# Kernel tuning notes

Hardware: AMD Instinct MI355X
Metric: run time of the kernel (lower is better)

## Reference

```python
import jax, jax.numpy as jnp
import numpy as np


def setup_inputs() -> dict:
    key = jax.random.key(0)
    k1, k2, k3, k4 = jax.random.split(key, 4)
    N, F_in, F_out = 8192, 512, 256
    inp = jax.random.normal(k1, (N, F_in), dtype=jnp.float32)
    adj = jax.random.uniform(k2, (N, N), dtype=jnp.float32)
    stdv = 1.0 / np.sqrt(F_out)
    weight = jax.random.uniform(k3, (F_in, F_out), minval=-stdv, maxval=stdv, dtype=jnp.float32)
    b = jax.random.uniform(k4, (F_out,), minval=-stdv, maxval=stdv, dtype=jnp.float32)
    return {"input": inp, "adj": adj, "weight": weight, "b": b}


def reference(input, adj, weight, b):
    N = adj.shape[0]
    degree = jnp.sum(adj, axis=1)                      # [N]
    # A_tilde = 2*I - adj
    A_tilde = 2.0 * jnp.eye(N, dtype=adj.dtype) - adj
    d_inv_sqrt = 1.0 / jnp.sqrt(2.0 + degree)          # [N]
    # D^-1/2 @ A_tilde @ D^-1/2 as broadcasted row/col scaling (same math, O(N^2))
    L_sharpen = d_inv_sqrt[:, None] * A_tilde * d_inv_sqrt[None, :]
    support = input @ weight                           # [N, F_out]
    out = L_sharpen @ support + b                      # [N, F_out]
    return jax.nn.relu(out)
```

## Files before the change

kernel.cpp:

```cpp
#include <hip/hip_runtime.h>


typedef _Float16 h4 __attribute__((ext_vector_type(4)));
typedef _Float16 h8 __attribute__((ext_vector_type(8)));
typedef float f4 __attribute__((ext_vector_type(4)));

__device__ __forceinline__ void gload_lds16(const void* g, void* l) {
    __builtin_amdgcn_global_load_lds(
        (const __attribute__((address_space(1))) void*)g,
        (__attribute__((address_space(3))) void*)l, 16, 0, 0);
}

__device__ __forceinline__ void gload2(const float* p, f4& x, f4& y) {
    asm volatile("global_load_dwordx4 %0, %2, off\n\t"
                 "global_load_dwordx4 %1, %2, off offset:16"
                 : "=&v"(x), "=&v"(y)
                 : "v"(p)
                 : "memory");
}
__device__ __forceinline__ void gloadB2(const char* p, h8& x, h8& y) {
    asm volatile("global_load_dwordx4 %0, %2, off\n\t"
                 "global_load_dwordx4 %1, %2, off offset:64"
                 : "=&v"(x), "=&v"(y)
                 : "v"(p)
                 : "memory");
}

__global__ __launch_bounds__(256) void k0_wt(const float* __restrict__ weight,
                                             char* __restrict__ wt) {
    const int idx = blockIdx.x * 256 + threadIdx.x;
    const int k = idx >> 8, j = idx & 255;
    const _Float16 h = (_Float16)weight[idx];
    const int off = j * 1024 + ((k >> 6) << 7) + (((k & 63) << 1) ^ ((j & 7) << 4));
    *(_Float16*)(wt + off) = h;
}

__global__ __launch_bounds__(256) void k1_deg(const float* __restrict__ adj,
                                              float* __restrict__ dinv) {
    const int r = blockIdx.x;
    const float4* rp = (const float4*)(adj + (size_t)r * 8192);
    const int t = threadIdx.x;
    float s = 0.f;
#pragma unroll
    for (int i = 0; i < 8; ++i) {
        float4 v = rp[t + i * 256];
        s += (v.x + v.y) + (v.z + v.w);
    }
#pragma unroll
    for (int off = 32; off > 0; off >>= 1) s += __shfl_down(s, off, 64);
    __shared__ float part[4];
    if ((t & 63) == 0) part[t >> 6] = s;
    __syncthreads();
    if (t == 0) {
        float deg = (part[0] + part[1]) + (part[2] + part[3]);
        dinv[r] = 1.0f / sqrtf(2.0f + deg);
    }
}

__global__ __launch_bounds__(512) void k2_support(const float* __restrict__ input,
                                                  const char* __restrict__ wt,
                                                  const float* __restrict__ dinv,
                                                  char* __restrict__ sT) {
    __shared__ char smem[4096 + 32768];
    const int t = threadIdx.x, w = t >> 6, l = t & 63;
    const int r0 = (int)blockIdx.x * 32;
    const int arow = t >> 4, ak4 = t & 15;
    const int bj = l >> 3, bb = (l & 7) * 16;

    f4 acc[2][2] = {};

    for (int kt = 0; kt < 8; ++kt) {
        const int k0 = kt * 64;
        __syncthreads();
        {
            float4 v = *(const float4*)(input + (size_t)(r0 + arow) * 512 + k0 + ak4 * 4);
            h4 h;
            h[0] = (_Float16)v.x; h[1] = (_Float16)v.y;
            h[2] = (_Float16)v.z; h[3] = (_Float16)v.w;
            *(h4*)(smem + arow * 128 + ((ak4 * 8) ^ ((arow & 7) << 4))) = h;
        }
#pragma unroll
        for (int q = 0; q < 4; ++q) {
            const int c = q * 8 + w;
            gload_lds16(wt + (size_t)(c * 8 + bj) * 1024 + kt * 128 + bb,
                        smem + 4096 + c * 1024);
        }
        __syncthreads();
#pragma unroll
        for (int kk = 0; kk < 2; ++kk) {
            const int ko = kk * 64 + ((l >> 4) << 4);
            h8 a[2], b[2];
#pragma unroll
            for (int m = 0; m < 2; ++m) {
                const int r = m * 16 + (l & 15);
                a[m] = *(const h8*)(smem + r * 128 + (ko ^ ((r & 7) << 4)));
            }
#pragma unroll
            for (int n = 0; n < 2; ++n) {
                const int j = w * 32 + n * 16 + (l & 15);
                b[n] = *(const h8*)(smem + 4096 + j * 128 + (ko ^ ((j & 7) << 4)));
            }
#pragma unroll
            for (int m = 0; m < 2; ++m)
#pragma unroll
                for (int n = 0; n < 2; ++n)
                    acc[m][n] = __builtin_amdgcn_mfma_f32_16x16x32_f16(a[m], b[n], acc[m][n], 0, 0, 0);
        }
    }
#pragma unroll
    for (int m = 0; m < 2; ++m)
#pragma unroll
        for (int n = 0; n < 2; ++n) {
            const int j = w * 32 + n * 16 + (l & 15);
            const int k0r = r0 + m * 16 + ((l >> 4) << 2);
            h4 h;
#pragma unroll
            for (int r = 0; r < 4; ++r)
                h[r] = (_Float16)(dinv[k0r + r] * acc[m][n][r]);
            *(h4*)(sT + (size_t)j * 16384 + (size_t)k0r * 2) = h;
        }
}

__global__ __launch_bounds__(512, 4) void k3_spmm(const float* __restrict__ adj,
                                                  const char* __restrict__ sT,
                                                  float* __restrict__ part,
                                                  float* __restrict__ out,
                                                  int steps) {
    __shared__ __align__(16) char smem[2][8192];
    const int t = threadIdx.x;
    const int w = t >> 6, l = t & 63;
    const int i0 = (int)blockIdx.x * 64;
    const int ks0 = (int)blockIdx.y * steps * 64;
    const int dkt = (i0 - ks0) >> 6;

    const int arow = t >> 3;
    const int ak8 = (t & 7) * 8;
    const int arow_g = i0 + arow;
    const float* aptr = adj + (size_t)arow_g * 8192 + ks0 + ak8;
    const int a_off = arow * 128 + (((t & 7) << 4) ^ ((arow & 7) << 4));

    const char* bp0 = sT + ((size_t)(w * 32 + (l & 15)) * 8192 + ks0 + ((l >> 4) << 3)) * 2;
    const char* bp1 = bp0 + (size_t)16 * 16384;

    f4 acc[4][2] = {};
    h8 bv[2][2];
    f4 ax0, ay0, ax1, ay1;

    auto loadB = [&](int kt) {
        gloadB2(bp0 + (size_t)kt * 128, bv[0][0], bv[1][0]);
        gloadB2(bp1 + (size_t)kt * 128, bv[0][1], bv[1][1]);
    };
    auto waitB = [&]() {
    };
    auto writeA = [&](char* buf, int kt, const f4 x, const f4 y) {
        const int kg = ks0 + kt * 64 + ak8;
        h8 h;
        if (kt == dkt) {
#pragma unroll
            for (int e = 0; e < 4; ++e)
                h[e] = (_Float16)((arow_g == kg + e) ? 2.0f - x[e] : -x[e]);
#pragma unroll
            for (int e = 0; e < 4; ++e)
                h[4 + e] = (_Float16)((arow_g == kg + 4 + e) ? 2.0f - y[e] : -y[e]);
        } else {
#pragma unroll
            for (int e = 0; e < 4; ++e) h[e] = (_Float16)(-x[e]);
#pragma unroll
            for (int e = 0; e < 4; ++e) h[4 + e] = (_Float16)(-y[e]);
        }
        *(h8*)(buf + a_off) = h;
    };
    auto compute = [&](const char* A) {
#pragma unroll
        for (int kk = 0; kk < 2; ++kk) {
            const int ko = kk * 64 + ((l >> 4) << 4);
            h8 a[4];
#pragma unroll
            for (int m = 0; m < 4; ++m) {
                const int r = m * 16 + (l & 15);
                a[m] = *(const h8*)(A + r * 128 + (ko ^ ((r & 7) << 4)));
            }
#pragma unroll
            for (int m = 0; m < 4; ++m)
#pragma unroll
                for (int n = 0; n < 2; ++n)
                    acc[m][n] = __builtin_amdgcn_mfma_f32_16x16x32_f16(a[m], bv[kk][n], acc[m][n], 0, 0, 0);
        }
    };

#define WAIT_ADJ(N, X, Y)                                                     \
    asm volatile("s_waitcnt vmcnt(" #N ")" : "+v"(X), "+v"(Y) :: "memory");   \
    __builtin_amdgcn_sched_barrier(0);
#define WAIT_B(N)                                                             \
    asm volatile("s_waitcnt vmcnt(" #N ")"                                    \
                 : "+v"(bv[0][0]), "+v"(bv[0][1]), "+v"(bv[1][0]), "+v"(bv[1][1]) \
                 :: "memory");                                                \
    __builtin_amdgcn_sched_barrier(0);
#define BARRIER()                                                             \
    asm volatile("s_waitcnt lgkmcnt(0)\n\ts_barrier" ::: "memory");           \
    __builtin_amdgcn_sched_barrier(0);

    gload2(aptr, ax0, ay0);
    gload2(aptr + 64, ax1, ay1);
    WAIT_ADJ(2, ax0, ay0)
    writeA(smem[0], 0, ax0, ay0);
    BARRIER()

#define BODY(kt, XC, YC, XN, YN, BUFC, BUFN)                                  \
    {                                                                         \
        loadB(kt);                                                            \
        gload2(aptr + (size_t)(kt + 2) * 64, XC, YC);                         \
        WAIT_ADJ(6, XN, YN)                                                   \
        writeA(BUFN, (kt) + 1, XN, YN);                                       \
        WAIT_B(2)                                                             \
        compute(BUFC);                                                        \
        BARRIER()                                                             \
    }

    for (int kt2 = 0; kt2 + 3 <= steps; kt2 += 2) {
        BODY(kt2,     ax0, ay0, ax1, ay1, smem[0], smem[1])
        BODY(kt2 + 1, ax1, ay1, ax0, ay0, smem[1], smem[0])
    }
    {
        loadB(steps - 2);
        WAIT_ADJ(4, ax1, ay1)
        writeA(smem[1], steps - 1, ax1, ay1);
        WAIT_B(0)
        compute(smem[0]);
        BARRIER()
    }
    {
        loadB(steps - 1);
        WAIT_B(0)
        compute(smem[1]);
    }
#undef BODY
#undef WAIT_ADJ
#undef WAIT_B
#undef BARRIER

    float* dst = (blockIdx.y == gridDim.y - 1) ? out
               : part + (size_t)blockIdx.y * (8192 * 256);
#pragma unroll
    for (int m = 0; m < 4; ++m)
#pragma unroll
        for (int n = 0; n < 2; ++n) {
            const int j = w * 32 + n * 16 + (l & 15);
            const int ib = i0 + m * 16 + ((l >> 4) << 2);
#pragma unroll
            for (int r = 0; r < 4; ++r)
                dst[(size_t)(ib + r) * 256 + j] = acc[m][n][r];
        }
}

__global__ __launch_bounds__(256) void k4_fin(const float* __restrict__ part,
                                              float* __restrict__ out,
                                              const float* __restrict__ dinv,
                                              const float* __restrict__ bias,
                                              int nsplit) {
    const int idx = blockIdx.x * 256 + threadIdx.x;
    float4 s = ((const float4*)out)[idx];
    for (int sp = 0; sp < nsplit - 1; ++sp)
        s += ((const float4*)(part + (size_t)sp * (8192 * 256)))[idx];
    const float dv = dinv[idx >> 6];
    const float4 b = ((const float4*)bias)[idx & 63];
    float4 r;
    r.x = fmaxf(dv * s.x + b.x, 0.f);
    r.y = fmaxf(dv * s.y + b.y, 0.f);
    r.z = fmaxf(dv * s.z + b.z, 0.f);
    r.w = fmaxf(dv * s.w + b.w, 0.f);
    ((float4*)out)[idx] = r;
}

extern "C" void kernel_launch(void* const* d_in, const int* in_sizes, int n_in,
                              void* d_out, int out_size, void* d_ws, size_t ws_size,
                              hipStream_t stream) {
    const float* input  = (const float*)d_in[0];
    const float* adj    = (const float*)d_in[1];
    const float* weight = (const float*)d_in[2];
    const float* bias   = (const float*)d_in[3];
    float* out = (float*)d_out;

    char* ws = (char*)d_ws;
    float* dinv = (float*)ws;
    char*  wt   = ws + 32768;
    char*  sT   = ws + 294912;
    float* part = (float*)(ws + 294912 + 4194304);

    const size_t base = 294912 + 4194304;
    int nsplit = 1;
    if (ws_size >= base + 3 * 8388608) nsplit = 4;
    else if (ws_size >= base + 1 * 8388608) nsplit = 2;
    const int steps = 128 / nsplit;

    k0_wt<<<512, 256, 0, stream>>>(weight, wt);
    k1_deg<<<8192, 256, 0, stream>>>(adj, dinv);
    k2_support<<<256, 512, 0, stream>>>(input, wt, dinv, sT);
    k3_spmm<<<dim3(128, nsplit), 512, 0, stream>>>(adj, sT, part, out, steps);
    k4_fin<<<2048, 256, 0, stream>>>(part, out, dinv, bias, nsplit);
}
```

Baseline: 149.6 us.

## Store support in MFMA-fragment layout and prefetch B one step ahead

The support matrix is now written in a blocked layout where each wavefront's B fragment for a k-step is a contiguous 1 KB chunk, so each lane loads 16 contiguous bytes. The loads are coalesced where before they were strided 16 KB row reads. B fragments are double-buffered in registers and loaded one k-step ahead, so compute no longer waits on a B load issued in the same step. The cost is extra VGPRs for the second B buffer, which could press occupancy at launch bounds of 512 threads with 4 blocks, and waitcnt accounting that must stay correct.

```diff
diff --git a/kernel.cpp b/kernel.cpp
--- a/kernel.cpp
+++ b/kernel.cpp
@@ -18,9 +18,9 @@
                  : "v"(p)
                  : "memory");
 }
-__device__ __forceinline__ void gloadB2(const char* p, h8& x, h8& y) {
+__device__ __forceinline__ void gloadBfrag(const char* p, h8& x, h8& y) {
     asm volatile("global_load_dwordx4 %0, %2, off\n\t"
-                 "global_load_dwordx4 %1, %2, off offset:64"
+                 "global_load_dwordx4 %1, %2, off offset:1024"
                  : "=&v"(x), "=&v"(y)
                  : "v"(p)
                  : "memory");
@@ -117,7 +117,11 @@
 #pragma unroll
             for (int r = 0; r < 4; ++r)
                 h[r] = (_Float16)(dinv[k0r + r] * acc[m][n][r]);
-            *(h4*)(sT + (size_t)j * 16384 + (size_t)k0r * 2) = h;
+            const int off = (((j >> 4) * 128 + (k0r >> 6)) << 11) +
+                            (((k0r >> 5) & 1) << 10) +
+                            ((((k0r >> 3) & 3) << 4) + (j & 15)) * 16 +
+                            ((k0r & 7) << 1);
+            *(h4*)(sT + off) = h;
         }
 }
 
@@ -139,18 +143,17 @@
     const float* aptr = adj + (size_t)arow_g * 8192 + ks0 + ak8;
     const int a_off = arow * 128 + (((t & 7) << 4) ^ ((arow & 7) << 4));
 
-    const char* bp0 = sT + ((size_t)(w * 32 + (l & 15)) * 8192 + ks0 + ((l >> 4) << 3)) * 2;
-    const char* bp1 = bp0 + (size_t)16 * 16384;
+    const int chunk0 = ks0 >> 6;
+    const char* bpn0 = sT + ((size_t)(w * 2) * 128 + chunk0) * 2048 + l * 16;
+    const char* bpn1 = bpn0 + 262144;
 
     f4 acc[4][2] = {};
-    h8 bv[2][2];
+    h8 bvA[2][2], bvB[2][2];
     f4 ax0, ay0, ax1, ay1;
 
-    auto loadB = [&](int kt) {
-        gloadB2(bp0 + (size_t)kt * 128, bv[0][0], bv[1][0]);
-        gloadB2(bp1 + (size_t)kt * 128, bv[0][1], bv[1][1]);
-    };
-    auto waitB = [&]() {
+    auto loadB = [&](int kt, h8 (&bv)[2][2]) {
+        gloadBfrag(bpn0 + (size_t)kt * 2048, bv[0][0], bv[1][0]);
+        gloadBfrag(bpn1 + (size_t)kt * 2048, bv[0][1], bv[1][1]);
     };
     auto writeA = [&](char* buf, int kt, const f4 x, const f4 y) {
         const int kg = ks0 + kt * 64 + ak8;
@@ -170,7 +173,7 @@
         }
         *(h8*)(buf + a_off) = h;
     };
-    auto compute = [&](const char* A) {
+    auto compute = [&](const char* A, const h8 (&bv)[2][2]) {
 #pragma unroll
         for (int kk = 0; kk < 2; ++kk) {
             const int ko = kk * 64 + ((l >> 4) << 4);
@@ -188,56 +191,62 @@
         }
     };
 
+#define SBAR0() __builtin_amdgcn_sched_barrier(0)
 #define WAIT_ADJ(N, X, Y)                                                     \
     asm volatile("s_waitcnt vmcnt(" #N ")" : "+v"(X), "+v"(Y) :: "memory");   \
-    __builtin_amdgcn_sched_barrier(0);
-#define WAIT_B(N)                                                             \
+    SBAR0();
+#define WAIT_STEP(N, X, Y, BV)                                                \
     asm volatile("s_waitcnt vmcnt(" #N ")"                                    \
-                 : "+v"(bv[0][0]), "+v"(bv[0][1]), "+v"(bv[1][0]), "+v"(bv[1][1]) \
-                 :: "memory");                                                \
-    __builtin_amdgcn_sched_barrier(0);
+                 : "+v"(X), "+v"(Y), "+v"(BV[0][0]), "+v"(BV[0][1]),          \
+                   "+v"(BV[1][0]), "+v"(BV[1][1]) :: "memory");               \
+    SBAR0();
+#define WAIT_BV(N, BV)                                                        \
+    asm volatile("s_waitcnt vmcnt(" #N ")"                                    \
+                 : "+v"(BV[0][0]), "+v"(BV[0][1]),                            \
+                   "+v"(BV[1][0]), "+v"(BV[1][1]) :: "memory");               \
+    SBAR0();
 #define BARRIER()                                                             \
     asm volatile("s_waitcnt lgkmcnt(0)\n\ts_barrier" ::: "memory");           \
-    __builtin_amdgcn_sched_barrier(0);
+    SBAR0();
 
     gload2(aptr, ax0, ay0);
+    loadB(0, bvA);
+    WAIT_ADJ(4, ax0, ay0)
+    writeA(smem[0], 0, ax0, ay0);
     gload2(aptr + 64, ax1, ay1);
-    WAIT_ADJ(2, ax0, ay0)
-    writeA(smem[0], 0, ax0, ay0);
     BARRIER()
 
-#define BODY(kt, XC, YC, XN, YN, BUFC, BUFN)                                  \
+#define BODY(kt, XC, YC, XN, YN, BVC, BVN, BUFC, BUFN)                        \
     {                                                                         \
-        loadB(kt);                                                            \
-        gload2(aptr + (size_t)(kt + 2) * 64, XC, YC);                         \
-        WAIT_ADJ(6, XN, YN)                                                   \
+        loadB((kt) + 1, BVN);                                                 \
+        gload2(aptr + (size_t)((kt) + 2) * 64, XC, YC);                       \
+        WAIT_STEP(6, XN, YN, BVC)                                             \
         writeA(BUFN, (kt) + 1, XN, YN);                                       \
-        WAIT_B(2)                                                             \
-        compute(BUFC);                                                        \
+        compute(BUFC, BVC);                                                   \
         BARRIER()                                                             \
     }
 
-    for (int kt2 = 0; kt2 + 3 <= steps; kt2 += 2) {
-        BODY(kt2,     ax0, ay0, ax1, ay1, smem[0], smem[1])
-        BODY(kt2 + 1, ax1, ay1, ax0, ay0, smem[1], smem[0])
+    for (int kt2 = 0; kt2 + 2 <= steps - 2; kt2 += 2) {
+        BODY(kt2,     ax0, ay0, ax1, ay1, bvA, bvB, smem[0], smem[1])
+        BODY(kt2 + 1, ax1, ay1, ax0, ay0, bvB, bvA, smem[1], smem[0])
     }
     {
-        loadB(steps - 2);
-        WAIT_ADJ(4, ax1, ay1)
+        loadB(steps - 1, bvB);
+        WAIT_STEP(4, ax1, ay1, bvA)
         writeA(smem[1], steps - 1, ax1, ay1);
-        WAIT_B(0)
-        compute(smem[0]);
+        compute(smem[0], bvA);
         BARRIER()
     }
     {
-        loadB(steps - 1);
-        WAIT_B(0)
-        compute(smem[1]);
+        WAIT_BV(0, bvB)
+        compute(smem[1], bvB);
     }
 #undef BODY
 #undef WAIT_ADJ
-#undef WAIT_B
+#undef WAIT_STEP
+#undef WAIT_BV
 #undef BARRIER
+#undef SBAR0
 
     float* dst = (blockIdx.y == gridDim.y - 1) ? out
                : part + (size_t)blockIdx.y * (8192 * 256);
```

Result: faster. 136.9 us (-8.5%).
